# Kernel tuning notes

Measured on AMD Instinct MI355X. Metric: run time of the kernel, lower is better.

Reference implementation:

```python
import jax, jax.numpy as jnp
import numpy as np

# Config (matches init_kwargs)
S = 8            # num_seqs
LQ = 256         # query tokens per sequence (num_tokens = S*LQ = 2048)
SEQ = 2048       # kv seq_len per sequence
BLK = 16         # block size
NBLK_PER_SEQ = SEQ // BLK   # 128 = max_num_blocks_per_seq
NUM_BLKS = S * NBLK_PER_SEQ # 1024
HQ = 32          # num_query_heads
HKV = 8          # num_kv_heads
G = HQ // HKV    # queries per kv head (GQA group)
D = 128          # head_size
WINDOW = 1024    # sliding_window
SCALE = 1.0 / float(np.sqrt(D))


def setup_inputs() -> dict:
    key = jax.random.key(0)
    k1, k2, k3 = jax.random.split(key, 3)
    query = jax.random.normal(k1, (S * LQ, HQ, D), jnp.float32)
    key_cache = jax.random.normal(k2, (NUM_BLKS, BLK, HKV, D), jnp.float32)
    value_cache = jax.random.normal(k3, (NUM_BLKS, BLK, HKV, D), jnp.float32)
    # each sequence owns a contiguous run of blocks; all indices valid (>=0)
    block_tables = jnp.arange(NUM_BLKS, dtype=jnp.int32).reshape(S, NBLK_PER_SEQ)
    seq_lens = jnp.full((S,), SEQ, dtype=jnp.int32)
    query_start_len = (jnp.arange(S + 1, dtype=jnp.int32) * LQ)
    return dict(query=query, key_cache=key_cache, value_cache=value_cache,
                block_tables=block_tables, seq_lens=seq_lens,
                query_start_len=query_start_len)


def reference(query, key_cache, value_cache, block_tables, seq_lens, query_start_len):
    # query: [S*LQ, HQ, D] -> [S, LQ, HKV, G, D]
    q = query.reshape(S, LQ, HKV, G, D)
    # paged KV gather: [S, NBLK_PER_SEQ] -> [S, NBLK_PER_SEQ, BLK, HKV, D] -> [S, SEQ, HKV, D]
    K = key_cache[block_tables].reshape(S, SEQ, HKV, D)
    V = value_cache[block_tables].reshape(S, SEQ, HKV, D)
    # attention scores: [S, HKV, G, LQ, SEQ]
    scores = jnp.einsum('sqhgd,skhd->shgqk', q, K) * SCALE
    # causal + sliding-window mask over absolute positions
    ctx = SEQ - LQ  # context_len (same for all seqs here)
    qpos = ctx + jnp.arange(LQ)          # [LQ] absolute query positions
    kpos = jnp.arange(SEQ)               # [SEQ] absolute key positions
    valid = (kpos[None, :] <= qpos[:, None]) & \
            (qpos[:, None] - kpos[None, :] < WINDOW)   # [LQ, SEQ]
    neg_inf = jnp.asarray(-jnp.inf, scores.dtype)
    scores = jnp.where(valid[None, None, None, :, :], scores, neg_inf)
    probs = jax.nn.softmax(scores, axis=-1)
    # output: [S, LQ, HKV, G, D] -> [S*LQ, HQ, D]
    out = jnp.einsum('shgqk,skhd->sqhgd', probs, V)
    return out.reshape(S * LQ, HQ, D)
```

## Files before the change

kernel.cpp:

```cpp
#include <hip/hip_runtime.h>
#include <stdint.h>

typedef __attribute__((ext_vector_type(8))) short short8;
typedef __attribute__((ext_vector_type(4))) float floatx4;
typedef __attribute__((ext_vector_type(16))) float f32x16;
typedef __attribute__((ext_vector_type(4))) unsigned int uint4v;

#define NSEQ 8
#define BLKSZ 16
#define NBLK_PER_SEQ 128
#define HQN 32
#define HKVN 8
#define GQ 4
#define HD 128
#define WINDOW 1024
#define SCALE 0.08838834764831845f

#define QB 32
#define KVB 32
#define KROW 136
#define VROW 40

#define MFMA32 __builtin_amdgcn_mfma_f32_32x32x16_bf16

static __device__ __forceinline__ unsigned int pack2bf(float lo, float hi) {
    unsigned int a = __builtin_bit_cast(unsigned int, lo) + 0x8000u;
    unsigned int b = __builtin_bit_cast(unsigned int, hi) + 0x8000u;
    return __builtin_amdgcn_perm(b, a, 0x07060302u);
}

__global__ __launch_bounds__(256, 2)
void attn_fwd(const float* __restrict__ qg,
              const float* __restrict__ kg,
              const float* __restrict__ vg,
              const int* __restrict__ bt,
              const int* __restrict__ seqlens,
              const int* __restrict__ qsl,
              float* __restrict__ outg)
{
    __shared__ __align__(16) short Klds[2][KVB][KROW];
    __shared__ __align__(16) short Vt[2][HD][VROW];

    const int tid  = threadIdx.x;
    const int lane = tid & 63;
    const int wave = tid >> 6;
    const int l31  = lane & 31;
    const int hi   = lane >> 5;

    const int b  = blockIdx.x;
    const int h  = b & 7;
    const int qt = (b >> 3) & 7;
    const int s  = b >> 6;
    const int q0 = qt * QB;

    const int qstart = qsl[s];
    const int numq   = qsl[s + 1] - qstart;
    const int slen   = seqlens[s];
    const int ctx    = slen - numq;
    const int hq     = h * GQ + wave;

    short8 qf[8];
    {
        const float* qrow = qg + ((size_t)(qstart + q0 + l31) * HQN + hq) * HD;
        #pragma unroll
        for (int ks = 0; ks < 8; ++ks) {
            floatx4 f0 = *(const floatx4*)(qrow + ks * 16 + hi * 8);
            floatx4 f1 = *(const floatx4*)(qrow + ks * 16 + hi * 8 + 4);
            uint4v w;
            w[0] = pack2bf(f0[0] * SCALE, f0[1] * SCALE);
            w[1] = pack2bf(f0[2] * SCALE, f0[3] * SCALE);
            w[2] = pack2bf(f1[0] * SCALE, f1[1] * SCALE);
            w[3] = pack2bf(f1[2] * SCALE, f1[3] * SCALE);
            qf[ks] = __builtin_bit_cast(short8, w);
        }
    }

    f32x16 oacc[4];
    #pragma unroll
    for (int dblk = 0; dblk < 4; ++dblk)
        #pragma unroll
        for (int i = 0; i < 16; ++i)
            oacc[dblk][i] = 0.f;

    float mrun = -INFINITY, lrun = 0.f;

    int lo = ctx + q0 - WINDOW + 1; if (lo < 0) lo = 0;
    int hiq = ctx + q0 + QB - 1;    if (hiq > slen - 1) hiq = slen - 1;
    const int t0 = lo / KVB, t1 = hiq / KVB;

    const int srow = tid >> 3;
    const int sd0  = (tid & 7) * 16;
    const int k2   = tid & 15;
    const int d0v  = (tid >> 4) * 8;

    floatx4 fk[4], fv[4];

#define LOAD_TILE(kv0_) {                                                            \
        const int kvp = (kv0_) + srow;                                               \
        const int blk = bt[s * NBLK_PER_SEQ + (kvp >> 4)];                           \
        const float* src = kg + (((size_t)blk * BLKSZ + (kvp & 15)) * HKVN + h) * HD + sd0; \
        fk[0] = *(const floatx4*)(src);                                              \
        fk[1] = *(const floatx4*)(src + 4);                                          \
        fk[2] = *(const floatx4*)(src + 8);                                          \
        fk[3] = *(const floatx4*)(src + 12);                                         \
        const int kvv = (kv0_) + 2 * k2;                                             \
        const int blkv = bt[s * NBLK_PER_SEQ + (kvv >> 4)];                          \
        const float* vsrc = vg + (((size_t)blkv * BLKSZ + (kvv & 15)) * HKVN + h) * HD + d0v; \
        fv[0] = *(const floatx4*)(vsrc);                                             \
        fv[1] = *(const floatx4*)(vsrc + 4);                                         \
        fv[2] = *(const floatx4*)(vsrc + (size_t)HKVN * HD);                         \
        fv[3] = *(const floatx4*)(vsrc + (size_t)HKVN * HD + 4);                     \
    }

    LOAD_TILE(t0 * KVB);

    int cur = 0;
    for (int t = t0; t <= t1; ++t) {
        const int kv0 = t * KVB;

        {
            uint4v w;
            w[0] = pack2bf(fk[0][0], fk[0][1]);
            w[1] = pack2bf(fk[0][2], fk[0][3]);
            w[2] = pack2bf(fk[1][0], fk[1][1]);
            w[3] = pack2bf(fk[1][2], fk[1][3]);
            *(uint4v*)&Klds[cur][srow][sd0] = w;
            w[0] = pack2bf(fk[2][0], fk[2][1]);
            w[1] = pack2bf(fk[2][2], fk[2][3]);
            w[2] = pack2bf(fk[3][0], fk[3][1]);
            w[3] = pack2bf(fk[3][2], fk[3][3]);
            *(uint4v*)&Klds[cur][srow][sd0 + 8] = w;
            #pragma unroll
            for (int i = 0; i < 8; ++i) {
                *(unsigned int*)&Vt[cur][d0v + i][2 * k2] =
                    pack2bf(fv[i >> 2][i & 3], fv[2 + (i >> 2)][i & 3]);
            }
        }

        if (t < t1) LOAD_TILE(kv0 + KVB);

        __syncthreads();

        f32x16 sacc;
        #pragma unroll
        for (int i = 0; i < 16; ++i) sacc[i] = 0.f;
        #pragma unroll
        for (int ks = 0; ks < 8; ++ks) {
            short8 kf = *(const short8*)&Klds[cur][l31][ks * 16 + hi * 8];
            sacc = MFMA32(kf, qf[ks], sacc, 0, 0, 0);
        }

        const bool interior = (kv0 >= ctx + q0 - (WINDOW - QB)) &&
                              (kv0 + KVB - 1 <= ctx + q0);
        const int qpos = ctx + q0 + l31;
        float p[16];
        float rmax = -INFINITY;
        #pragma unroll
        for (int r = 0; r < 16; ++r) {
            float x = sacc[r];
            if (!interior) {
                const int kpos = kv0 + (r & 3) + 4 * hi + 8 * (r >> 2);
                const bool valid = (kpos <= qpos) && (qpos - kpos < WINDOW);
                x = valid ? x : -INFINITY;
            }
            p[r] = x;
            rmax = fmaxf(rmax, x);
        }
        rmax = fmaxf(rmax, __shfl_xor(rmax, 32));
        const float mold = mrun;
        const bool defer = __all(rmax <= mold + 8.0f);
        const float mnew = defer ? mold : fmaxf(mold, rmax);
        const float alpha = defer ? 1.0f
            : ((mold == -INFINITY) ? ((mnew == -INFINITY) ? 1.0f : 0.0f)
                                   : __expf(mold - mnew));
        const bool dead = (mnew == -INFINITY);
        float rsum = 0.f;
        #pragma unroll
        for (int r = 0; r < 16; ++r) {
            float e = dead ? 0.f : __expf(p[r] - mnew);
            p[r] = e;
            rsum += e;
        }
        rsum += __shfl_xor(rsum, 32);
        lrun = lrun * alpha + rsum;
        mrun = mnew;
        if (!defer) {
            #pragma unroll
            for (int dblk = 0; dblk < 4; ++dblk)
                oacc[dblk] = oacc[dblk] * alpha;
        }

        unsigned int c0 = pack2bf(p[0],  p[1]);
        unsigned int c1 = pack2bf(p[2],  p[3]);
        unsigned int c2 = pack2bf(p[4],  p[5]);
        unsigned int c3 = pack2bf(p[6],  p[7]);
        unsigned int c4 = pack2bf(p[8],  p[9]);
        unsigned int c5 = pack2bf(p[10], p[11]);
        unsigned int c6 = pack2bf(p[12], p[13]);
        unsigned int c7 = pack2bf(p[14], p[15]);
        unsigned int o0 = (unsigned int)__shfl_xor((int)c0, 32);
        unsigned int o1 = (unsigned int)__shfl_xor((int)c1, 32);
        unsigned int o2 = (unsigned int)__shfl_xor((int)c2, 32);
        unsigned int o3 = (unsigned int)__shfl_xor((int)c3, 32);
        unsigned int o4 = (unsigned int)__shfl_xor((int)c4, 32);
        unsigned int o5 = (unsigned int)__shfl_xor((int)c5, 32);
        unsigned int o6 = (unsigned int)__shfl_xor((int)c6, 32);
        unsigned int o7 = (unsigned int)__shfl_xor((int)c7, 32);
        uint4v u0, u1;
        u0[0] = hi ? o2 : c0;
        u0[1] = hi ? o3 : c1;
        u0[2] = hi ? c2 : o0;
        u0[3] = hi ? c3 : o1;
        u1[0] = hi ? o6 : c4;
        u1[1] = hi ? o7 : c5;
        u1[2] = hi ? c6 : o4;
        u1[3] = hi ? c7 : o5;
        short8 pb0 = __builtin_bit_cast(short8, u0);
        short8 pb1 = __builtin_bit_cast(short8, u1);

        #pragma unroll
        for (int dblk = 0; dblk < 4; ++dblk) {
            short8 vf0 = *(const short8*)&Vt[cur][dblk * 32 + l31][hi * 8];
            short8 vf1 = *(const short8*)&Vt[cur][dblk * 32 + l31][16 + hi * 8];
            oacc[dblk] = MFMA32(vf0, pb0, oacc[dblk], 0, 0, 0);
            oacc[dblk] = MFMA32(vf1, pb1, oacc[dblk], 0, 0, 0);
        }

        cur ^= 1;
    }
#undef LOAD_TILE

    {
        const float inv = 1.0f / lrun;
        float* orow = outg + ((size_t)(qstart + q0 + l31) * HQN + hq) * HD;
        #pragma unroll
        for (int dblk = 0; dblk < 4; ++dblk) {
            #pragma unroll
            for (int rq = 0; rq < 4; ++rq) {
                floatx4 o;
                o[0] = oacc[dblk][4 * rq + 0] * inv;
                o[1] = oacc[dblk][4 * rq + 1] * inv;
                o[2] = oacc[dblk][4 * rq + 2] * inv;
                o[3] = oacc[dblk][4 * rq + 3] * inv;
                *(floatx4*)(orow + dblk * 32 + 8 * rq + 4 * hi) = o;
            }
        }
    }
}

extern "C" void kernel_launch(void* const* d_in, const int* in_sizes, int n_in,
                              void* d_out, int out_size, void* d_ws, size_t ws_size,
                              hipStream_t stream) {
    const float* q  = (const float*)d_in[0];
    const float* k  = (const float*)d_in[1];
    const float* v  = (const float*)d_in[2];
    const int* btp  = (const int*)d_in[3];
    const int* sl   = (const int*)d_in[4];
    const int* qs   = (const int*)d_in[5];
    float* out      = (float*)d_out;

    attn_fwd<<<dim3(NSEQ * HKVN * 8), 256, 0, stream>>>(q, k, v, btp, sl, qs, out);
}
```

Measured before the change: 85.15 us.

## Double KV tile to 64, single-buffer K with extra barrier, use exp2 softmax

Raises the KV tile from 32 to 64 keys, so each iteration issues two QK MFMAs per k-step and twice the PV MFMAs. This halves the number of loop iterations, barriers and softmax reductions. K is now single-buffered, with a second __syncthreads after the QK MFMAs to protect it, while V stays double-buffered. The query is prescaled by scale*log2(e) so the softmax can use exp2f, and the defer threshold is rescaled to match. The costs are higher register pressure from 8 prefetched float4 K/V vectors and the extra barrier, which could hurt occupancy at launch_bounds(256,2).

```diff
diff --git a/kernel.cpp b/kernel.cpp
--- a/kernel.cpp
+++ b/kernel.cpp
@@ -14,12 +14,12 @@
 #define GQ 4
 #define HD 128
 #define WINDOW 1024
-#define SCALE 0.08838834764831845f
+#define QSCALE 0.12751744f
 
 #define QB 32
-#define KVB 32
+#define KVB 64
 #define KROW 136
-#define VROW 40
+#define VROW 72
 
 #define MFMA32 __builtin_amdgcn_mfma_f32_32x32x16_bf16
 
@@ -38,7 +38,7 @@
               const int* __restrict__ qsl,
               float* __restrict__ outg)
 {
-    __shared__ __align__(16) short Klds[2][KVB][KROW];
+    __shared__ __align__(16) short Klds[KVB][KROW];
     __shared__ __align__(16) short Vt[2][HD][VROW];
 
     const int tid  = threadIdx.x;
@@ -67,10 +67,10 @@
             floatx4 f0 = *(const floatx4*)(qrow + ks * 16 + hi * 8);
             floatx4 f1 = *(const floatx4*)(qrow + ks * 16 + hi * 8 + 4);
             uint4v w;
-            w[0] = pack2bf(f0[0] * SCALE, f0[1] * SCALE);
-            w[1] = pack2bf(f0[2] * SCALE, f0[3] * SCALE);
-            w[2] = pack2bf(f1[0] * SCALE, f1[1] * SCALE);
-            w[3] = pack2bf(f1[2] * SCALE, f1[3] * SCALE);
+            w[0] = pack2bf(f0[0] * QSCALE, f0[1] * QSCALE);
+            w[1] = pack2bf(f0[2] * QSCALE, f0[3] * QSCALE);
+            w[2] = pack2bf(f1[0] * QSCALE, f1[1] * QSCALE);
+            w[3] = pack2bf(f1[2] * QSCALE, f1[3] * QSCALE);
             qf[ks] = __builtin_bit_cast(short8, w);
         }
     }
@@ -93,94 +93,108 @@
     const int k2   = tid & 15;
     const int d0v  = (tid >> 4) * 8;
 
-    floatx4 fk[4], fv[4];
-
-#define LOAD_TILE(kv0_) {                                                            \
-        const int kvp = (kv0_) + srow;                                               \
+    floatx4 fk[8], fv[8];
+
+#define LOAD_HALF(kv0_, p) {                                                         \
+        const int kvp = (kv0_) + (p) * 32 + srow;                                    \
         const int blk = bt[s * NBLK_PER_SEQ + (kvp >> 4)];                           \
         const float* src = kg + (((size_t)blk * BLKSZ + (kvp & 15)) * HKVN + h) * HD + sd0; \
-        fk[0] = *(const floatx4*)(src);                                              \
-        fk[1] = *(const floatx4*)(src + 4);                                          \
-        fk[2] = *(const floatx4*)(src + 8);                                          \
-        fk[3] = *(const floatx4*)(src + 12);                                         \
-        const int kvv = (kv0_) + 2 * k2;                                             \
+        fk[(p)*4+0] = *(const floatx4*)(src);                                        \
+        fk[(p)*4+1] = *(const floatx4*)(src + 4);                                    \
+        fk[(p)*4+2] = *(const floatx4*)(src + 8);                                    \
+        fk[(p)*4+3] = *(const floatx4*)(src + 12);                                   \
+        const int kvv = (kv0_) + (p) * 32 + 2 * k2;                                  \
         const int blkv = bt[s * NBLK_PER_SEQ + (kvv >> 4)];                          \
         const float* vsrc = vg + (((size_t)blkv * BLKSZ + (kvv & 15)) * HKVN + h) * HD + d0v; \
-        fv[0] = *(const floatx4*)(vsrc);                                             \
-        fv[1] = *(const floatx4*)(vsrc + 4);                                         \
-        fv[2] = *(const floatx4*)(vsrc + (size_t)HKVN * HD);                         \
-        fv[3] = *(const floatx4*)(vsrc + (size_t)HKVN * HD + 4);                     \
-    }
+        fv[(p)*4+0] = *(const floatx4*)(vsrc);                                       \
+        fv[(p)*4+1] = *(const floatx4*)(vsrc + 4);                                   \
+        fv[(p)*4+2] = *(const floatx4*)(vsrc + (size_t)HKVN * HD);                   \
+        fv[(p)*4+3] = *(const floatx4*)(vsrc + (size_t)HKVN * HD + 4);               \
+    }
+#define LOAD_TILE(kv0_) { LOAD_HALF(kv0_, 0); LOAD_HALF(kv0_, 1); }
 
     LOAD_TILE(t0 * KVB);
 
-    int cur = 0;
     for (int t = t0; t <= t1; ++t) {
         const int kv0 = t * KVB;
-
-        {
+        const int vb  = t & 1;
+
+        #pragma unroll
+        for (int p = 0; p < 2; ++p) {
+            const int row = p * 32 + srow;
             uint4v w;
-            w[0] = pack2bf(fk[0][0], fk[0][1]);
-            w[1] = pack2bf(fk[0][2], fk[0][3]);
-            w[2] = pack2bf(fk[1][0], fk[1][1]);
-            w[3] = pack2bf(fk[1][2], fk[1][3]);
-            *(uint4v*)&Klds[cur][srow][sd0] = w;
-            w[0] = pack2bf(fk[2][0], fk[2][1]);
-            w[1] = pack2bf(fk[2][2], fk[2][3]);
-            w[2] = pack2bf(fk[3][0], fk[3][1]);
-            w[3] = pack2bf(fk[3][2], fk[3][3]);
-            *(uint4v*)&Klds[cur][srow][sd0 + 8] = w;
+            w[0] = pack2bf(fk[p*4+0][0], fk[p*4+0][1]);
+            w[1] = pack2bf(fk[p*4+0][2], fk[p*4+0][3]);
+            w[2] = pack2bf(fk[p*4+1][0], fk[p*4+1][1]);
+            w[3] = pack2bf(fk[p*4+1][2], fk[p*4+1][3]);
+            *(uint4v*)&Klds[row][sd0] = w;
+            w[0] = pack2bf(fk[p*4+2][0], fk[p*4+2][1]);
+            w[1] = pack2bf(fk[p*4+2][2], fk[p*4+2][3]);
+            w[2] = pack2bf(fk[p*4+3][0], fk[p*4+3][1]);
+            w[3] = pack2bf(fk[p*4+3][2], fk[p*4+3][3]);
+            *(uint4v*)&Klds[row][sd0 + 8] = w;
+        }
+        #pragma unroll
+        for (int p = 0; p < 2; ++p)
             #pragma unroll
             for (int i = 0; i < 8; ++i) {
-                *(unsigned int*)&Vt[cur][d0v + i][2 * k2] =
-                    pack2bf(fv[i >> 2][i & 3], fv[2 + (i >> 2)][i & 3]);
-            }
-        }
+                *(unsigned int*)&Vt[vb][d0v + i][p * 32 + 2 * k2] =
+                    pack2bf(fv[p*4 + (i >> 2)][i & 3], fv[p*4 + 2 + (i >> 2)][i & 3]);
+            }
 
         if (t < t1) LOAD_TILE(kv0 + KVB);
 
         __syncthreads();
 
-        f32x16 sacc;
-        #pragma unroll
-        for (int i = 0; i < 16; ++i) sacc[i] = 0.f;
+        f32x16 sacc0, sacc1;
+        #pragma unroll
+        for (int i = 0; i < 16; ++i) { sacc0[i] = 0.f; sacc1[i] = 0.f; }
         #pragma unroll
         for (int ks = 0; ks < 8; ++ks) {
-            short8 kf = *(const short8*)&Klds[cur][l31][ks * 16 + hi * 8];
-            sacc = MFMA32(kf, qf[ks], sacc, 0, 0, 0);
-        }
+            short8 kf0 = *(const short8*)&Klds[l31][ks * 16 + hi * 8];
+            short8 kf1 = *(const short8*)&Klds[32 + l31][ks * 16 + hi * 8];
+            sacc0 = MFMA32(kf0, qf[ks], sacc0, 0, 0, 0);
+            sacc1 = MFMA32(kf1, qf[ks], sacc1, 0, 0, 0);
+        }
+
+        __syncthreads();
 
         const bool interior = (kv0 >= ctx + q0 - (WINDOW - QB)) &&
                               (kv0 + KVB - 1 <= ctx + q0);
         const int qpos = ctx + q0 + l31;
-        float p[16];
+        float p2[2][16];
         float rmax = -INFINITY;
         #pragma unroll
-        for (int r = 0; r < 16; ++r) {
-            float x = sacc[r];
-            if (!interior) {
-                const int kpos = kv0 + (r & 3) + 4 * hi + 8 * (r >> 2);
-                const bool valid = (kpos <= qpos) && (qpos - kpos < WINDOW);
-                x = valid ? x : -INFINITY;
-            }
-            p[r] = x;
-            rmax = fmaxf(rmax, x);
+        for (int m2 = 0; m2 < 2; ++m2) {
+            #pragma unroll
+            for (int r = 0; r < 16; ++r) {
+                float x = (m2 == 0) ? sacc0[r] : sacc1[r];
+                if (!interior) {
+                    const int kpos = kv0 + m2 * 32 + (r & 3) + 4 * hi + 8 * (r >> 2);
+                    const bool valid = (kpos <= qpos) && (qpos - kpos < WINDOW);
+                    x = valid ? x : -INFINITY;
+                }
+                p2[m2][r] = x;
+                rmax = fmaxf(rmax, x);
+            }
         }
         rmax = fmaxf(rmax, __shfl_xor(rmax, 32));
         const float mold = mrun;
-        const bool defer = __all(rmax <= mold + 8.0f);
+        const bool defer = __all(rmax <= mold + 11.0f);
         const float mnew = defer ? mold : fmaxf(mold, rmax);
         const float alpha = defer ? 1.0f
             : ((mold == -INFINITY) ? ((mnew == -INFINITY) ? 1.0f : 0.0f)
-                                   : __expf(mold - mnew));
+                                   : exp2f(mold - mnew));
         const bool dead = (mnew == -INFINITY);
         float rsum = 0.f;
         #pragma unroll
-        for (int r = 0; r < 16; ++r) {
-            float e = dead ? 0.f : __expf(p[r] - mnew);
-            p[r] = e;
-            rsum += e;
-        }
+        for (int m2 = 0; m2 < 2; ++m2)
+            #pragma unroll
+            for (int r = 0; r < 16; ++r) {
+                float e = dead ? 0.f : exp2f(p2[m2][r] - mnew);
+                p2[m2][r] = e;
+                rsum += e;
+            }
         rsum += __shfl_xor(rsum, 32);
         lrun = lrun * alpha + rsum;
         mrun = mnew;
@@ -190,45 +204,51 @@
                 oacc[dblk] = oacc[dblk] * alpha;
         }
 
-        unsigned int c0 = pack2bf(p[0],  p[1]);
-        unsigned int c1 = pack2bf(p[2],  p[3]);
-        unsigned int c2 = pack2bf(p[4],  p[5]);
-        unsigned int c3 = pack2bf(p[6],  p[7]);
-        unsigned int c4 = pack2bf(p[8],  p[9]);
-        unsigned int c5 = pack2bf(p[10], p[11]);
-        unsigned int c6 = pack2bf(p[12], p[13]);
-        unsigned int c7 = pack2bf(p[14], p[15]);
-        unsigned int o0 = (unsigned int)__shfl_xor((int)c0, 32);
-        unsigned int o1 = (unsigned int)__shfl_xor((int)c1, 32);
-        unsigned int o2 = (unsigned int)__shfl_xor((int)c2, 32);
-        unsigned int o3 = (unsigned int)__shfl_xor((int)c3, 32);
-        unsigned int o4 = (unsigned int)__shfl_xor((int)c4, 32);
-        unsigned int o5 = (unsigned int)__shfl_xor((int)c5, 32);
-        unsigned int o6 = (unsigned int)__shfl_xor((int)c6, 32);
-        unsigned int o7 = (unsigned int)__shfl_xor((int)c7, 32);
-        uint4v u0, u1;
-        u0[0] = hi ? o2 : c0;
-        u0[1] = hi ? o3 : c1;
-        u0[2] = hi ? c2 : o0;
-        u0[3] = hi ? c3 : o1;
-        u1[0] = hi ? o6 : c4;
-        u1[1] = hi ? o7 : c5;
-        u1[2] = hi ? c6 : o4;
-        u1[3] = hi ? c7 : o5;
-        short8 pb0 = __builtin_bit_cast(short8, u0);
-        short8 pb1 = __builtin_bit_cast(short8, u1);
-
-        #pragma unroll
-        for (int dblk = 0; dblk < 4; ++dblk) {
-            short8 vf0 = *(const short8*)&Vt[cur][dblk * 32 + l31][hi * 8];
-            short8 vf1 = *(const short8*)&Vt[cur][dblk * 32 + l31][16 + hi * 8];
-            oacc[dblk] = MFMA32(vf0, pb0, oacc[dblk], 0, 0, 0);
-            oacc[dblk] = MFMA32(vf1, pb1, oacc[dblk], 0, 0, 0);
-        }
-
-        cur ^= 1;
+        short8 pb[2][2];
+        #pragma unroll
+        for (int m2 = 0; m2 < 2; ++m2) {
+            unsigned int c0 = pack2bf(p2[m2][0],  p2[m2][1]);
+            unsigned int c1 = pack2bf(p2[m2][2],  p2[m2][3]);
+            unsigned int c2 = pack2bf(p2[m2][4],  p2[m2][5]);
+            unsigned int c3 = pack2bf(p2[m2][6],  p2[m2][7]);
+            unsigned int c4 = pack2bf(p2[m2][8],  p2[m2][9]);
+            unsigned int c5 = pack2bf(p2[m2][10], p2[m2][11]);
+            unsigned int c6 = pack2bf(p2[m2][12], p2[m2][13]);
+            unsigned int c7 = pack2bf(p2[m2][14], p2[m2][15]);
+            unsigned int o0 = (unsigned int)__shfl_xor((int)c0, 32);
+            unsigned int o1 = (unsigned int)__shfl_xor((int)c1, 32);
+            unsigned int o2 = (unsigned int)__shfl_xor((int)c2, 32);
+            unsigned int o3 = (unsigned int)__shfl_xor((int)c3, 32);
+            unsigned int o4 = (unsigned int)__shfl_xor((int)c4, 32);
+            unsigned int o5 = (unsigned int)__shfl_xor((int)c5, 32);
+            unsigned int o6 = (unsigned int)__shfl_xor((int)c6, 32);
+            unsigned int o7 = (unsigned int)__shfl_xor((int)c7, 32);
+            uint4v u0, u1;
+            u0[0] = hi ? o2 : c0;
+            u0[1] = hi ? o3 : c1;
+            u0[2] = hi ? c2 : o0;
+            u0[3] = hi ? c3 : o1;
+            u1[0] = hi ? o6 : c4;
+            u1[1] = hi ? o7 : c5;
+            u1[2] = hi ? c6 : o4;
+            u1[3] = hi ? c7 : o5;
+            pb[m2][0] = __builtin_bit_cast(short8, u0);
+            pb[m2][1] = __builtin_bit_cast(short8, u1);
+        }
+
+        #pragma unroll
+        for (int m2 = 0; m2 < 2; ++m2) {
+            #pragma unroll
+            for (int dblk = 0; dblk < 4; ++dblk) {
+                short8 vf0 = *(const short8*)&Vt[vb][dblk * 32 + l31][m2 * 32 + hi * 8];
+                short8 vf1 = *(const short8*)&Vt[vb][dblk * 32 + l31][m2 * 32 + 16 + hi * 8];
+                oacc[dblk] = MFMA32(vf0, pb[m2][0], oacc[dblk], 0, 0, 0);
+                oacc[dblk] = MFMA32(vf1, pb[m2][1], oacc[dblk], 0, 0, 0);
+            }
+        }
     }
 #undef LOAD_TILE
+#undef LOAD_HALF
 
     {
         const float inv = 1.0f / lrun;
```

Result: faster. 79.69 us (-6.4%).
